# Optimization experiments

Hardware: AMD Instinct MI355X
Metric: run time of the kernel (lower is better)

## Reference

```python
import jax, jax.numpy as jnp
import numpy as np

EMBED = 1024  # embed_dim = hidden_dim = out_dim (n_head=1)
NQ, NK = 4096, 4096
NEG = 1e16


def setup_inputs() -> dict:
    key = jax.random.key(0)
    ks = jax.random.split(key, 10)
    stdv = 1.0 / np.sqrt(EMBED)
    lin = lambda kk: jax.random.uniform(kk, (EMBED, EMBED), jnp.float32, -stdv, stdv)
    vec = lambda kk: jax.random.uniform(kk, (EMBED,), jnp.float32, -stdv, stdv)
    return {
        "q": jax.random.normal(ks[0], (NQ, EMBED), jnp.float32),
        "k": jax.random.normal(ks[1], (NK, EMBED), jnp.float32),
        "mask": jax.random.randint(ks[2], (NQ, NK), 0, 2, jnp.int32),
        "wei": jax.random.uniform(ks[3], (NQ, NK), jnp.float32),
        "Wq": lin(ks[4]), "bq": vec(ks[5]),
        "Wk": lin(ks[6]), "bk": vec(ks[7]),
        "Wp": lin(ks[8]), "bp": vec(ks[9]),
    }


def reference(q, k, mask, wei, Wq, bq, Wk, bk, Wp, bp):
    # Linear projections (torch Linear: x @ W.T + b)
    kx = k @ Wk.T + bk                      # [NK, D]
    qx = q @ Wq.T + bq                      # [NQ, D]
    # dot_product score
    score = qx @ kx.T                       # [NQ, NK]
    bias = (mask.astype(jnp.int32) - 1).astype(score.dtype) * NEG
    score = jax.nn.softmax(score + bias, axis=-1)
    # second weighted+masked softmax pass
    score = jax.nn.softmax(score * wei + bias, axis=-1)
    out = (score @ kx) @ Wp.T + bp          # [NQ, D]
    return out, score
```

## Files before the change

kernel.cpp:

```cpp
#include <hip/hip_runtime.h>


typedef __bf16 bf16;
typedef __bf16 bf16x8 __attribute__((ext_vector_type(8)));
typedef __bf16 bf16x4 __attribute__((ext_vector_type(4)));
typedef float  f32x4  __attribute__((ext_vector_type(4)));
typedef float  f32x16 __attribute__((ext_vector_type(16)));
typedef int    i32x4  __attribute__((ext_vector_type(4)));

typedef __attribute__((address_space(1))) void as1_void;
typedef __attribute__((address_space(3))) void as3_void;

#define NQ  4096
#define NKK 4096
#define EMB 1024

#define BM 128
#define BN 128
#define BK 32

__device__ __forceinline__ void gld_lds16(const void* g, void* l) {
    __builtin_amdgcn_global_load_lds((as1_void*)g, (as3_void*)l, 16, 0, 0);
}

__global__ __launch_bounds__(256) void prep_all(
    const float* __restrict__ q, const float* __restrict__ k,
    const float* __restrict__ Wq, const float* __restrict__ Wk, const float* __restrict__ Wp,
    bf16* __restrict__ qh, bf16* __restrict__ ql,
    bf16* __restrict__ kh, bf16* __restrict__ kl,
    bf16* __restrict__ Wqh, bf16* __restrict__ Wql,
    bf16* __restrict__ Wkh, bf16* __restrict__ Wkl,
    bf16* __restrict__ Wph, bf16* __restrict__ Wpl,
    int nqk, int nw)
{
    const int z = blockIdx.y;
    const float* s; bf16* h; bf16* l; int n;
    switch (z) {
        case 0:  s = q;  h = qh;  l = ql;  n = nqk; break;
        case 1:  s = k;  h = kh;  l = kl;  n = nqk; break;
        case 2:  s = Wq; h = Wqh; l = Wql; n = nw;  break;
        case 3:  s = Wk; h = Wkh; l = Wkl; n = nw;  break;
        default: s = Wp; h = Wph; l = Wpl; n = nw;  break;
    }
    const int i = (blockIdx.x * 256 + threadIdx.x) * 4;
    if (i >= n) return;
    f32x4 v = *(const f32x4*)(s + i);
    bf16x4 hv, lv;
#pragma unroll
    for (int c = 0; c < 4; c++) {
        float x = v[c];
        bf16 hh = (bf16)x;
        hv[c] = hh;
        lv[c] = (bf16)(x - (float)hh);
    }
    *(bf16x4*)(h + i) = hv;
    *(bf16x4*)(l + i) = lv;
}

template<int NS, int MODE>
__global__ __launch_bounds__(256) void reduce_k(
    const float* __restrict__ P, const float* __restrict__ bias,
    float* __restrict__ of, bf16* __restrict__ oh, int n, int Nld)
{
    const int i = (blockIdx.x * 256 + threadIdx.x) * 4;
    if (i >= n) return;
    f32x4 v = *(const f32x4*)(P + i);
#pragma unroll
    for (int s = 1; s < NS; s++)
        v += *(const f32x4*)(P + (size_t)s * n + i);
    if (MODE == 1)
        v += *(const f32x4*)(bias + (i & (Nld - 1)));
    if (MODE == 0) {
        bf16x4 o;
#pragma unroll
        for (int c = 0; c < 4; c++) o[c] = (bf16)v[c];
        *(bf16x4*)(oh + i) = o;
    } else {
        *(f32x4*)(of + i) = v;
    }
}

template<int NSPLIT, int HAS_BIAS, int OUT_BF16>
__global__ __launch_bounds__(256) void gemm_bt(
    const bf16* __restrict__ A, const bf16* __restrict__ B,
    const float* __restrict__ bias,
    float* __restrict__ Cf, bf16* __restrict__ Cb,
    int M, int N, int Ksub, int lda, int ldb)
{
    __shared__ bf16 sA[BM * BK];
    __shared__ bf16 sB[BN * BK];
    const int t    = threadIdx.x;
    const int wave = t >> 6;
    const int lane = t & 63;
    const int l31  = lane & 31;
    const int lhi  = lane >> 5;
    const int wm   = wave >> 1;
    const int wn   = wave & 1;
    const int bm   = blockIdx.y * BM;
    const int bn   = blockIdx.x * BN;
    const int srow = t >> 2;
    const int gseg = (t & 3) ^ ((srow >> 1) & 3) ^ ((srow >> 3) & 3);
    const int rsw  = ((l31 >> 1) & 3) ^ ((l31 >> 3) & 3);
    const int kz   = (NSPLIT > 0) ? (int)blockIdx.z : 0;

    A += (size_t)kz * Ksub;
    B += (size_t)kz * Ksub;
    if (NSPLIT > 0) Cf += (size_t)kz * M * N;

    const bf16* ga = A + (size_t)(bm + srow) * lda + gseg * 8;
    const bf16* gb = B + (size_t)(bn + srow) * ldb + gseg * 8;
    char* lA = (char*)sA + wave * 1024;
    char* lB = (char*)sB + wave * 1024;

    f32x16 acc[2][2] = {};

    for (int k0 = 0; k0 < Ksub; k0 += BK) {
        __syncthreads();
        gld_lds16(ga + k0,                      lA);
        gld_lds16(ga + (size_t)64 * lda + k0,   lA + 4096);
        gld_lds16(gb + k0,                      lB);
        gld_lds16(gb + (size_t)64 * ldb + k0,   lB + 4096);
        __syncthreads();
        bf16x8 af[2][2], bfr[2][2];
#pragma unroll
        for (int mi = 0; mi < 2; mi++)
#pragma unroll
            for (int kh = 0; kh < 2; kh++)
                af[mi][kh] = *(const bf16x8*)
                    &sA[(wm * 64 + mi * 32 + l31) * BK + ((kh * 2 + lhi) ^ rsw) * 8];
#pragma unroll
        for (int nj = 0; nj < 2; nj++)
#pragma unroll
            for (int kh = 0; kh < 2; kh++)
                bfr[nj][kh] = *(const bf16x8*)
                    &sB[(wn * 64 + nj * 32 + l31) * BK + ((kh * 2 + lhi) ^ rsw) * 8];
#pragma unroll
        for (int kh = 0; kh < 2; kh++)
#pragma unroll
            for (int mi = 0; mi < 2; mi++)
#pragma unroll
                for (int nj = 0; nj < 2; nj++)
                    acc[mi][nj] = __builtin_amdgcn_mfma_f32_32x32x16_bf16(
                        af[mi][kh], bfr[nj][kh], acc[mi][nj], 0, 0, 0);
    }

#pragma unroll
    for (int mi = 0; mi < 2; mi++)
#pragma unroll
        for (int nj = 0; nj < 2; nj++) {
            const int cg = bn + wn * 64 + nj * 32 + l31;
            const float bv = HAS_BIAS ? bias[cg] : 0.0f;
#pragma unroll
            for (int r = 0; r < 16; r++) {
                const int rg = bm + wm * 64 + mi * 32 + (r & 3) + 8 * (r >> 2) + 4 * lhi;
                const float v = acc[mi][nj][r] + bv;
                const size_t idx = (size_t)rg * N + cg;
                if (NSPLIT > 0)    Cf[idx] = v;
                else if (OUT_BF16) Cb[idx] = (bf16)v;
                else               Cf[idx] = v;
            }
        }
}

template<int BATCH, int HAS_BIAS, int HILO>
__global__ __launch_bounds__(256) void gemm_bt_split(
    const bf16* __restrict__ Ah0, const bf16* __restrict__ Al0,
    const bf16* __restrict__ Bh0, const bf16* __restrict__ Bl0,
    const float* __restrict__ bias0, bf16* __restrict__ Ch0, bf16* __restrict__ Cl0,
    const bf16* __restrict__ Ah1, const bf16* __restrict__ Al1,
    const bf16* __restrict__ Bh1, const bf16* __restrict__ Bl1,
    const float* __restrict__ bias1, bf16* __restrict__ Ch1, bf16* __restrict__ Cl1,
    float* __restrict__ Cf,
    int M, int N, int K)
{
    __shared__ bf16 sAh[BM * BK], sAl[BM * BK], sBh[BN * BK], sBl[BN * BK];
    const int t    = threadIdx.x;
    const int wave = t >> 6;
    const int lane = t & 63;
    const int l31  = lane & 31;
    const int lhi  = lane >> 5;
    const int wm   = wave >> 1;
    const int wn   = wave & 1;
    const int bm   = blockIdx.y * BM;
    const int bn   = blockIdx.x * BN;
    const int srow = t >> 2;
    const int gseg = (t & 3) ^ ((srow >> 1) & 3) ^ ((srow >> 3) & 3);
    const int rsw  = ((l31 >> 1) & 3) ^ ((l31 >> 3) & 3);

    const int mt = BATCH ? (int)blockIdx.z : 0;

    const bf16* Ah = (BATCH && mt) ? Ah1 : Ah0;
    const bf16* Al = (BATCH && mt) ? Al1 : Al0;
    const bf16* Bh = (BATCH && mt) ? Bh1 : Bh0;
    const bf16* Bl = (BATCH && mt) ? Bl1 : Bl0;
    const float* bias = (BATCH && mt) ? bias1 : bias0;
    bf16* Ch = (BATCH && mt) ? Ch1 : Ch0;
    bf16* Cl = (BATCH && mt) ? Cl1 : Cl0;

    const size_t offA = (size_t)(bm + srow) * K + gseg * 8;
    const size_t offB = (size_t)(bn + srow) * K + gseg * 8;
    char* lAh = (char*)sAh + wave * 1024;
    char* lAl = (char*)sAl + wave * 1024;
    char* lBh = (char*)sBh + wave * 1024;
    char* lBl = (char*)sBl + wave * 1024;

    f32x16 acc[2][2] = {};

    for (int k0 = 0; k0 < K; k0 += BK) {
        __syncthreads();
        gld_lds16(Ah + offA + k0,                  lAh);
        gld_lds16(Ah + offA + (size_t)64 * K + k0, lAh + 4096);
        gld_lds16(Al + offA + k0,                  lAl);
        gld_lds16(Al + offA + (size_t)64 * K + k0, lAl + 4096);
        gld_lds16(Bh + offB + k0,                  lBh);
        gld_lds16(Bh + offB + (size_t)64 * K + k0, lBh + 4096);
        gld_lds16(Bl + offB + k0,                  lBl);
        gld_lds16(Bl + offB + (size_t)64 * K + k0, lBl + 4096);
        __syncthreads();
#pragma unroll
        for (int kh = 0; kh < 2; kh++) {
            const int ksw = ((kh * 2 + lhi) ^ rsw) * 8;
            bf16x8 ah[2], al[2], bh2[2], bl2[2];
#pragma unroll
            for (int mi = 0; mi < 2; mi++) {
                const int ro = (wm * 64 + mi * 32 + l31) * BK + ksw;
                ah[mi] = *(const bf16x8*)&sAh[ro];
                al[mi] = *(const bf16x8*)&sAl[ro];
            }
#pragma unroll
            for (int nj = 0; nj < 2; nj++) {
                const int ro = (wn * 64 + nj * 32 + l31) * BK + ksw;
                bh2[nj] = *(const bf16x8*)&sBh[ro];
                bl2[nj] = *(const bf16x8*)&sBl[ro];
            }
#pragma unroll
            for (int mi = 0; mi < 2; mi++)
#pragma unroll
                for (int nj = 0; nj < 2; nj++) {
                    acc[mi][nj] = __builtin_amdgcn_mfma_f32_32x32x16_bf16(al[mi], bh2[nj], acc[mi][nj], 0, 0, 0);
                    acc[mi][nj] = __builtin_amdgcn_mfma_f32_32x32x16_bf16(ah[mi], bl2[nj], acc[mi][nj], 0, 0, 0);
                    acc[mi][nj] = __builtin_amdgcn_mfma_f32_32x32x16_bf16(ah[mi], bh2[nj], acc[mi][nj], 0, 0, 0);
                }
        }
    }

#pragma unroll
    for (int mi = 0; mi < 2; mi++)
#pragma unroll
        for (int nj = 0; nj < 2; nj++) {
            const int cg = bn + wn * 64 + nj * 32 + l31;
            const float bv = HAS_BIAS ? bias[cg] : 0.0f;
#pragma unroll
            for (int r = 0; r < 16; r++) {
                const int rg = bm + wm * 64 + mi * 32 + (r & 3) + 8 * (r >> 2) + 4 * lhi;
                const float v = acc[mi][nj][r] + bv;
                const size_t idx = (size_t)rg * N + cg;
                if (HILO) {
                    const bf16 hh = (bf16)v;
                    Ch[idx] = hh;
                    Cl[idx] = (bf16)(v - (float)hh);
                } else {
                    Cf[idx] = v;
                }
            }
        }
}

__global__ __launch_bounds__(512, 2) void gemm_score256(
    const bf16* __restrict__ Ah, const bf16* __restrict__ Al,
    const bf16* __restrict__ Bh, const bf16* __restrict__ Bl,
    float* __restrict__ Cf,
    const bf16* __restrict__ Wp, const bf16* __restrict__ Kx,
    bf16* __restrict__ kxpT)
{
    __shared__ bf16 smem[65536];
    const int t    = threadIdx.x;
    const int wave = t >> 6;
    const int lane = t & 63;
    const int l31  = lane & 31;
    const int lhi  = lane >> 5;
    const int wm   = wave >> 2;
    const int wn   = wave & 3;
    const int bm   = (blockIdx.x >> 4) * 256;
    const int bn   = (blockIdx.x & 15) * 256;
    const int K    = EMB;

    const int strow = wave * 32 + (lane >> 1);
    const int stcol = (lane & 1) * 8;
    const bf16* gAh = Ah + (size_t)(bm + strow) * K + stcol;
    const bf16* gAl = Al + (size_t)(bm + strow) * K + stcol;
    const bf16* gBh = Bh + (size_t)(bn + strow) * K + stcol;
    const bf16* gBl = Bl + (size_t)(bn + strow) * K + stcol;

    auto stage = [&](int sbB, int tt) {
        char* L = (char*)smem + sbB + wave * 1024;
        const int ko = tt * 16;
        gld_lds16(gAh + ko, L);
        gld_lds16(gAl + ko, L + 8192);
        gld_lds16(gBh + ko, L + 16384);
        gld_lds16(gBl + ko, L + 24576);
    };

    f32x16 acc[4][2] = {};

    const int aoff = (wm * 128 + l31) * 16 + lhi * 8;
    const int boff = 8192 + (wn * 64 + l31) * 16 + lhi * 8;

    auto tile_body = [&](int cbE, int sbB, int stt, bool do_stage) {
        __builtin_amdgcn_s_barrier();
        if (do_stage) stage(sbB, stt);
        bf16x8 a_h[4], a_l[4], b_h[2], b_l[2];
#pragma unroll
        for (int mi = 0; mi < 4; mi++) {
            a_h[mi] = *(const bf16x8*)&smem[cbE + aoff + mi * 512];
            a_l[mi] = *(const bf16x8*)&smem[cbE + 4096 + aoff + mi * 512];
        }
#pragma unroll
        for (int nj = 0; nj < 2; nj++) {
            b_h[nj] = *(const bf16x8*)&smem[cbE + boff + nj * 512];
            b_l[nj] = *(const bf16x8*)&smem[cbE + 4096 + boff + nj * 512];
        }
        asm volatile("s_waitcnt lgkmcnt(0)" ::: "memory");
        __builtin_amdgcn_sched_barrier(0);
        __builtin_amdgcn_s_setprio(1);
#pragma unroll
        for (int mi = 0; mi < 4; mi++)
#pragma unroll
            for (int nj = 0; nj < 2; nj++) {
                acc[mi][nj] = __builtin_amdgcn_mfma_f32_32x32x16_bf16(a_l[mi], b_h[nj], acc[mi][nj], 0, 0, 0);
                acc[mi][nj] = __builtin_amdgcn_mfma_f32_32x32x16_bf16(a_h[mi], b_l[nj], acc[mi][nj], 0, 0, 0);
                acc[mi][nj] = __builtin_amdgcn_mfma_f32_32x32x16_bf16(a_h[mi], b_h[nj], acc[mi][nj], 0, 0, 0);
            }
        __builtin_amdgcn_s_setprio(0);
    };

#define VW8 asm volatile("s_waitcnt vmcnt(8)" ::: "memory")
#define VW4 asm volatile("s_waitcnt vmcnt(4)" ::: "memory")
#define VW0 asm volatile("s_waitcnt vmcnt(0)" ::: "memory")

    stage(0, 0); stage(32768, 1); stage(65536, 2);

    for (int tb = 0; tb < 60; tb += 4) {
        VW8; tile_body(    0,  98304, tb + 3, true);
        VW8; tile_body(16384,      0, tb + 4, true);
        VW8; tile_body(32768,  32768, tb + 5, true);
        VW8; tile_body(49152,  65536, tb + 6, true);
    }
    VW8; tile_body(    0,  98304, 63, true);
    VW8; tile_body(16384,      0,  0, false);
    VW4; tile_body(32768,      0,  0, false);
    VW0; tile_body(49152,      0,  0, false);

#undef VW8
#undef VW4
#undef VW0

#pragma unroll
    for (int mi = 0; mi < 4; mi++)
#pragma unroll
        for (int nj = 0; nj < 2; nj++) {
            const int cg = bn + wn * 64 + nj * 32 + l31;
#pragma unroll
            for (int r = 0; r < 16; r++) {
                const int rg = bm + wm * 128 + mi * 32 + (r & 3) + 8 * (r >> 2) + 4 * lhi;
                Cf[(size_t)rg * NKK + cg] = acc[mi][nj][r];
            }
        }

    {
        const int srow = t >> 2;
        const int gseg = (t & 3) ^ ((srow >> 1) & 3) ^ ((srow >> 3) & 3);
        const int rsw  = ((l31 >> 1) & 3) ^ ((l31 >> 3) & 3);
        const int km  = (blockIdx.x >> 5) * 128;
        const int kn2 = (blockIdx.x & 31) * 128;
        const int wm4 = wave >> 1;
        const int wn2 = wave & 1;
        const int NT2 = K / BK;
        const bf16* gW = Wp + (size_t)(km  + srow) * K + gseg * 8;
        const bf16* gX = Kx + (size_t)(kn2 + srow) * K + gseg * 8;
        auto stageK = [&](int buf, int k0) {
            char* L = (char*)smem + buf * 16384 + wave * 1024;
            gld_lds16(gW + k0, L);
            gld_lds16(gX + k0, L + 8192);
        };
        f32x16 ac2[2] = {};
        stageK(0, 0);
        for (int it = 0; it < NT2; ++it) {
            const int cur = it & 1;
            const int cb  = cur * 8192;
            if (it < NT2 - 1) {
                stageK(cur ^ 1, (it + 1) * BK);
                asm volatile("s_waitcnt vmcnt(2)" ::: "memory");
            } else {
                asm volatile("s_waitcnt vmcnt(0)" ::: "memory");
            }
            __builtin_amdgcn_s_barrier();
#pragma unroll
            for (int kh = 0; kh < 2; kh++) {
                const int ksw = ((kh * 2 + lhi) ^ rsw) * 8;
                bf16x8 av  = *(const bf16x8*)&smem[cb + (wm4 * 32 + l31) * BK + ksw];
                bf16x8 bv0 = *(const bf16x8*)&smem[cb + 4096 + (wn2 * 64 + l31) * BK + ksw];
                bf16x8 bv1 = *(const bf16x8*)&smem[cb + 4096 + (wn2 * 64 + 32 + l31) * BK + ksw];
                ac2[0] = __builtin_amdgcn_mfma_f32_32x32x16_bf16(av, bv0, ac2[0], 0, 0, 0);
                ac2[1] = __builtin_amdgcn_mfma_f32_32x32x16_bf16(av, bv1, ac2[1], 0, 0, 0);
            }
            asm volatile("s_waitcnt lgkmcnt(0)" ::: "memory");
            __builtin_amdgcn_s_barrier();
        }
#pragma unroll
        for (int nj = 0; nj < 2; nj++) {
            const int cg = kn2 + wn2 * 64 + nj * 32 + l31;
#pragma unroll
            for (int r = 0; r < 16; r++) {
                const int rg = km + wm4 * 32 + (r & 3) + 8 * (r >> 2) + 4 * lhi;
                kxpT[(size_t)rg * NKK + cg] = (bf16)ac2[nj][r];
            }
        }
    }
}

__device__ __forceinline__ float wred_max(float v) {
#pragma unroll
    for (int off = 32; off > 0; off >>= 1) v = fmaxf(v, __shfl_xor(v, off));
    return v;
}
__device__ __forceinline__ float wred_sum(float v) {
#pragma unroll
    for (int off = 32; off > 0; off >>= 1) v += __shfl_xor(v, off);
    return v;
}

__global__ __launch_bounds__(256) void softmax2_kernel(
    float* __restrict__ score, const int* __restrict__ mask,
    const float* __restrict__ wei, bf16* __restrict__ scoreb)
{
    __shared__ float sred[4];
    const int row = blockIdx.x;
    const int t   = threadIdx.x;
    const size_t base = (size_t)row * NKK + (size_t)t * 16;
    const int wv = t >> 6, ln = t & 63;

    float l[16], w[16];
    unsigned mb = 0;
#pragma unroll
    for (int c = 0; c < 4; c++) {
        *(f32x4*)(l + 4 * c) = *(const f32x4*)(score + base + 4 * c);
        *(f32x4*)(w + 4 * c) = *(const f32x4*)(wei + base + 4 * c);
        i32x4 mv = *(const i32x4*)(mask + base + 4 * c);
#pragma unroll
        for (int j = 0; j < 4; j++) if (mv[j] != 0) mb |= 1u << (4 * c + j);
    }

    float mx = -__builtin_inff();
#pragma unroll
    for (int s = 0; s < 16; s++) if (mb & (1u << s)) mx = fmaxf(mx, l[s]);
    mx = wred_max(mx);
    if (ln == 0) sred[wv] = mx;
    __syncthreads();
    mx = fmaxf(fmaxf(sred[0], sred[1]), fmaxf(sred[2], sred[3]));
    __syncthreads();
    float sum = 0.f;
#pragma unroll
    for (int s = 0; s < 16; s++) {
        const float e = (mb & (1u << s)) ? __expf(l[s] - mx) : 0.f;
        l[s] = e; sum += e;
    }
    sum = wred_sum(sum);
    if (ln == 0) sred[wv] = sum;
    __syncthreads();
    sum = sred[0] + sred[1] + sred[2] + sred[3];
    __syncthreads();
    const float inv1 = 1.0f / sum;

#pragma unroll
    for (int s = 0; s < 16; s++) l[s] = l[s] * inv1 * w[s];

    float mx2 = -__builtin_inff();
#pragma unroll
    for (int s = 0; s < 16; s++) if (mb & (1u << s)) mx2 = fmaxf(mx2, l[s]);
    mx2 = wred_max(mx2);
    if (ln == 0) sred[wv] = mx2;
    __syncthreads();
    mx2 = fmaxf(fmaxf(sred[0], sred[1]), fmaxf(sred[2], sred[3]));
    __syncthreads();
    float sum2 = 0.f;
#pragma unroll
    for (int s = 0; s < 16; s++) {
        const float e = (mb & (1u << s)) ? __expf(l[s] - mx2) : 0.f;
        l[s] = e; sum2 += e;
    }
    sum2 = wred_sum(sum2);
    if (ln == 0) sred[wv] = sum2;
    __syncthreads();
    sum2 = sred[0] + sred[1] + sred[2] + sred[3];
    const float inv2 = 1.0f / sum2;

#pragma unroll
    for (int c = 0; c < 4; c++) {
        f32x4 pv;
#pragma unroll
        for (int j = 0; j < 4; j++) pv[j] = l[4 * c + j] * inv2;
        __builtin_nontemporal_store(pv, (f32x4*)(score + base + 4 * c));
#pragma unroll
        for (int j = 0; j < 4; j++) l[4 * c + j] = pv[j];
    }
    bf16x8 b0, b1;
#pragma unroll
    for (int j = 0; j < 8; j++) { b0[j] = (bf16)l[j]; b1[j] = (bf16)l[8 + j]; }
    *(bf16x8*)(scoreb + base)     = b0;
    *(bf16x8*)(scoreb + base + 8) = b1;
}

extern "C" void kernel_launch(void* const* d_in, const int* in_sizes, int n_in,
                              void* d_out, int out_size, void* d_ws, size_t ws_size,
                              hipStream_t stream)
{
    (void)in_sizes; (void)n_in; (void)out_size;
    const float* q    = (const float*)d_in[0];
    const float* k    = (const float*)d_in[1];
    const int*   mask = (const int*)  d_in[2];
    const float* wei  = (const float*)d_in[3];
    const float* Wq   = (const float*)d_in[4];
    const float* bq   = (const float*)d_in[5];
    const float* Wk   = (const float*)d_in[6];
    const float* bk   = (const float*)d_in[7];
    const float* Wp   = (const float*)d_in[8];
    const float* bp   = (const float*)d_in[9];

    float* out   = (float*)d_out;
    float* score = (float*)d_out + (size_t)NQ * EMB;

    char* ws = (char*)d_ws;
    size_t off = 0;
    auto alloc = [&](size_t bytes) -> char* {
        char* p = ws + off; off += (bytes + 255) & ~(size_t)255; return p;
    };
    const size_t n_qk = (size_t)NQ * EMB;
    const size_t n_w  = (size_t)EMB * EMB;
    const size_t n_sc = (size_t)NQ * NKK;

    bf16* qh   = (bf16*)alloc(n_qk * 2);
    bf16* ql   = (bf16*)alloc(n_qk * 2);
    bf16* kh   = (bf16*)alloc(n_qk * 2);
    bf16* kl   = (bf16*)alloc(n_qk * 2);
    bf16* qxh  = (bf16*)alloc(n_qk * 2);
    bf16* qxl  = (bf16*)alloc(n_qk * 2);
    bf16* kxh  = (bf16*)alloc(n_qk * 2);
    bf16* kxl  = (bf16*)alloc(n_qk * 2);
    bf16* Wqh  = (bf16*)alloc(n_w * 2);
    bf16* Wql  = (bf16*)alloc(n_w * 2);
    bf16* Wkh  = (bf16*)alloc(n_w * 2);
    bf16* Wkl  = (bf16*)alloc(n_w * 2);
    bf16* Wpb  = (bf16*)alloc(n_w * 2);
    bf16* Wpl  = (bf16*)alloc(n_w * 2);
    bf16* kxpTb = (bf16*)alloc(n_qk * 2);
    bf16* scoreb = (bf16*)alloc(n_sc * 2);
    const size_t base_off = off;
    float* P = (float*)alloc(2 * n_qk * 4);
    const bool ws_ok = (off <= ws_size);
    if (base_off > ws_size) return;

    const int MN = (int)n_qk;

    prep_all<<<dim3(n_qk / 1024, 5), 256, 0, stream>>>(
        q, k, Wq, Wk, Wp,
        qh, ql, kh, kl, Wqh, Wql, Wkh, Wkl, Wpb, Wpl,
        (int)n_qk, (int)n_w);

    gemm_bt_split<1, 1, 1><<<dim3(EMB / BN, NQ / BM, 2), 256, 0, stream>>>(
        qh, ql, Wqh, Wql, bq, qxh, qxl,
        kh, kl, Wkh, Wkl, bk, kxh, kxl,
        nullptr, NQ, EMB, EMB);

    gemm_score256<<<dim3(256), 512, 0, stream>>>(
        qxh, qxl, kxh, kxl, score, Wpb, kxh, kxpTb);

    softmax2_kernel<<<dim3(NQ), 256, 0, stream>>>(score, mask, wei, scoreb);

    if (ws_ok) {
        gemm_bt<2, 0, 0><<<dim3(EMB / BN, NQ / BM, 2), 256, 0, stream>>>(
            scoreb, kxpTb, nullptr, P, nullptr, NQ, EMB, NKK / 2, NKK, NKK);
        reduce_k<2, 1><<<dim3(MN / 1024), 256, 0, stream>>>(
            P, bp, out, nullptr, MN, EMB);
    } else {
        gemm_bt<0, 1, 0><<<dim3(EMB / BN, NQ / BM), 256, 0, stream>>>(
            scoreb, kxpTb, bp, out, nullptr, NQ, EMB, NKK, NKK, NKK);
    }
}
```

Measured before the change: 485.0 us.

## Stage operands in MFMA-fragment layout and deepen Wp·Kx pipeline to four buffers

```diff
diff --git a/kernel.cpp b/kernel.cpp
--- a/kernel.cpp
+++ b/kernel.cpp
@@ -22,6 +22,8 @@
 __device__ __forceinline__ void gld_lds16(const void* g, void* l) {
     __builtin_amdgcn_global_load_lds((as1_void*)g, (as3_void*)l, 16, 0, 0);
 }
+
+#define VWAIT(N) asm volatile("s_waitcnt vmcnt(" #N ")" ::: "memory")
 
 __global__ __launch_bounds__(256) void prep_all(
     const float* __restrict__ q, const float* __restrict__ k,
@@ -285,12 +287,11 @@
     const int bn   = (blockIdx.x & 15) * 256;
     const int K    = EMB;
 
-    const int strow = wave * 32 + (lane >> 1);
-    const int stcol = (lane & 1) * 8;
-    const bf16* gAh = Ah + (size_t)(bm + strow) * K + stcol;
-    const bf16* gAl = Al + (size_t)(bm + strow) * K + stcol;
-    const bf16* gBh = Bh + (size_t)(bn + strow) * K + stcol;
-    const bf16* gBl = Bl + (size_t)(bn + strow) * K + stcol;
+    const int strow = wave * 32 + l31;
+    const bf16* gAh = Ah + (size_t)(bm + strow) * K + lhi * 8;
+    const bf16* gAl = Al + (size_t)(bm + strow) * K + lhi * 8;
+    const bf16* gBh = Bh + (size_t)(bn + strow) * K + lhi * 8;
+    const bf16* gBl = Bl + (size_t)(bn + strow) * K + lhi * 8;
 
     auto stage = [&](int sbB, int tt) {
         char* L = (char*)smem + sbB + wave * 1024;
@@ -303,8 +304,8 @@
 
     f32x16 acc[4][2] = {};
 
-    const int aoff = (wm * 128 + l31) * 16 + lhi * 8;
-    const int boff = 8192 + (wn * 64 + l31) * 16 + lhi * 8;
+    const int aoff = wm * 4 * 512 + lhi * 256 + l31 * 8;
+    const int boff = 8192 + wn * 2 * 512 + lhi * 256 + l31 * 8;
 
     auto tile_body = [&](int cbE, int sbB, int stt, bool do_stage) {
         __builtin_amdgcn_s_barrier();
@@ -334,26 +335,18 @@
         __builtin_amdgcn_s_setprio(0);
     };
 
-#define VW8 asm volatile("s_waitcnt vmcnt(8)" ::: "memory")
-#define VW4 asm volatile("s_waitcnt vmcnt(4)" ::: "memory")
-#define VW0 asm volatile("s_waitcnt vmcnt(0)" ::: "memory")
-
     stage(0, 0); stage(32768, 1); stage(65536, 2);
 
     for (int tb = 0; tb < 60; tb += 4) {
-        VW8; tile_body(    0,  98304, tb + 3, true);
-        VW8; tile_body(16384,      0, tb + 4, true);
-        VW8; tile_body(32768,  32768, tb + 5, true);
-        VW8; tile_body(49152,  65536, tb + 6, true);
-    }
-    VW8; tile_body(    0,  98304, 63, true);
-    VW8; tile_body(16384,      0,  0, false);
-    VW4; tile_body(32768,      0,  0, false);
-    VW0; tile_body(49152,      0,  0, false);
-
-#undef VW8
-#undef VW4
-#undef VW0
+        VWAIT(8); tile_body(    0,  98304, tb + 3, true);
+        VWAIT(8); tile_body(16384,      0, tb + 4, true);
+        VWAIT(8); tile_body(32768,  32768, tb + 5, true);
+        VWAIT(8); tile_body(49152,  65536, tb + 6, true);
+    }
+    VWAIT(8); tile_body(    0,  98304, 63, true);
+    VWAIT(8); tile_body(16384,      0,  0, false);
+    VWAIT(4); tile_body(32768,      0,  0, false);
+    VWAIT(0); tile_body(49152,      0,  0, false);
 
 #pragma unroll
     for (int mi = 0; mi < 4; mi++)
@@ -368,45 +361,46 @@
         }
 
     {
-        const int srow = t >> 2;
-        const int gseg = (t & 3) ^ ((srow >> 1) & 3) ^ ((srow >> 3) & 3);
-        const int rsw  = ((l31 >> 1) & 3) ^ ((l31 >> 3) & 3);
         const int km  = (blockIdx.x >> 5) * 128;
         const int kn2 = (blockIdx.x & 31) * 128;
         const int wm4 = wave >> 1;
         const int wn2 = wave & 1;
-        const int NT2 = K / BK;
-        const bf16* gW = Wp + (size_t)(km  + srow) * K + gseg * 8;
-        const bf16* gX = Kx + (size_t)(kn2 + srow) * K + gseg * 8;
-        auto stageK = [&](int buf, int k0) {
-            char* L = (char*)smem + buf * 16384 + wave * 1024;
-            gld_lds16(gW + k0, L);
-            gld_lds16(gX + k0, L + 8192);
+        const bool isW = wave < 4;
+        const int wr = (wave & 3) * 32 + l31;
+        const bf16* gSrc = isW ? (Wp + (size_t)(km  + wr) * K + lhi * 8)
+                               : (Kx + (size_t)(kn2 + wr) * K + lhi * 8);
+        const int dstoff = (isW ? 0 : 4096) + (wave & 3) * 1024;
+        auto stageK = [&](int bufByte, int tt) {
+            gld_lds16(gSrc + tt * 16, (char*)smem + bufByte + dstoff);
         };
+        const int avoff = wm4 * 512 + lhi * 256 + l31 * 8;
+        const int bvoff = 2048 + wn2 * 2 * 512 + lhi * 256 + l31 * 8;
         f32x16 ac2[2] = {};
-        stageK(0, 0);
-        for (int it = 0; it < NT2; ++it) {
-            const int cur = it & 1;
-            const int cb  = cur * 8192;
-            if (it < NT2 - 1) {
-                stageK(cur ^ 1, (it + 1) * BK);
-                asm volatile("s_waitcnt vmcnt(2)" ::: "memory");
-            } else {
-                asm volatile("s_waitcnt vmcnt(0)" ::: "memory");
-            }
+
+        auto kbody = [&](int cbE, int bufByte, int stt, bool do_stage) {
             __builtin_amdgcn_s_barrier();
-#pragma unroll
-            for (int kh = 0; kh < 2; kh++) {
-                const int ksw = ((kh * 2 + lhi) ^ rsw) * 8;
-                bf16x8 av  = *(const bf16x8*)&smem[cb + (wm4 * 32 + l31) * BK + ksw];
-                bf16x8 bv0 = *(const bf16x8*)&smem[cb + 4096 + (wn2 * 64 + l31) * BK + ksw];
-                bf16x8 bv1 = *(const bf16x8*)&smem[cb + 4096 + (wn2 * 64 + 32 + l31) * BK + ksw];
-                ac2[0] = __builtin_amdgcn_mfma_f32_32x32x16_bf16(av, bv0, ac2[0], 0, 0, 0);
-                ac2[1] = __builtin_amdgcn_mfma_f32_32x32x16_bf16(av, bv1, ac2[1], 0, 0, 0);
-            }
+            if (do_stage) stageK(bufByte, stt);
+            bf16x8 av  = *(const bf16x8*)&smem[cbE + avoff];
+            bf16x8 bv0 = *(const bf16x8*)&smem[cbE + bvoff];
+            bf16x8 bv1 = *(const bf16x8*)&smem[cbE + bvoff + 512];
             asm volatile("s_waitcnt lgkmcnt(0)" ::: "memory");
-            __builtin_amdgcn_s_barrier();
-        }
+            __builtin_amdgcn_sched_barrier(0);
+            ac2[0] = __builtin_amdgcn_mfma_f32_32x32x16_bf16(av, bv0, ac2[0], 0, 0, 0);
+            ac2[1] = __builtin_amdgcn_mfma_f32_32x32x16_bf16(av, bv1, ac2[1], 0, 0, 0);
+        };
+
+        stageK(0, 0); stageK(8192, 1); stageK(16384, 2);
+        for (int tb = 0; tb < 60; tb += 4) {
+            VWAIT(2); kbody(    0, 24576, tb + 3, true);
+            VWAIT(2); kbody( 4096,     0, tb + 4, true);
+            VWAIT(2); kbody( 8192,  8192, tb + 5, true);
+            VWAIT(2); kbody(12288, 16384, tb + 6, true);
+        }
+        VWAIT(2); kbody(    0, 24576, 63, true);
+        VWAIT(2); kbody( 4096,     0,  0, false);
+        VWAIT(1); kbody( 8192,     0,  0, false);
+        VWAIT(0); kbody(12288,     0,  0, false);
+
 #pragma unroll
         for (int nj = 0; nj < 2; nj++) {
             const int cg = kn2 + wn2 * 64 + nj * 32 + l31;
```

Measured after the change: 485.7 us. No clear change (+0.1%).
